# Kernel tuning notes

Hardware: AMD Instinct MI355X
Metric: run time of the kernel (lower is better)

The kernel has to match this reference:

```python
import jax, jax.numpy as jnp
import numpy as np

# yolov5 non_max_suppression defaults (from forward's input_parameters.get defaults)
CONF_THRES = 0.25
IOU_THRES = 0.45
MAX_DET = 1000        # max detections returned per image
TOP_K = 4096          # fixed candidate count entering greedy NMS (jit-friendly stand-in for max_nms)
MAX_WH = 7680.0       # per-class box offset so NMS is class-aware (yolov5 trick)


def setup_inputs() -> dict:
    key = jax.random.key(0)
    k1, k2, k3, k4 = jax.random.split(key, 4)
    B, N, NC = 16, 25200, 80  # 640x640 yolov5 -> 25200 anchors, 80 COCO classes
    xy = jax.random.uniform(k1, (B, N, 2)) * 640.0            # box centers in pixels
    wh = jax.random.uniform(k2, (B, N, 2)) * 160.0 + 4.0       # box sizes
    obj = jax.random.uniform(k3, (B, N, 1))                    # objectness
    cls = jax.random.uniform(k4, (B, N, NC))                   # class scores
    pred = jnp.concatenate([xy, wh, obj, cls], axis=-1)        # [B, N, 85]
    return {"pred": pred}


def _xywh2xyxy(x):
    xy, wh = x[..., :2], x[..., 2:4]
    return jnp.concatenate([xy - wh * 0.5, xy + wh * 0.5], axis=-1)


def _iou_one_vs_all(box, boxes):
    # box [4], boxes [K,4], xyxy
    lt = jnp.maximum(box[:2], boxes[:, :2])
    rb = jnp.minimum(box[2:], boxes[:, 2:])
    wh = jnp.clip(rb - lt, 0.0)
    inter = wh[:, 0] * wh[:, 1]
    a1 = (box[2] - box[0]) * (box[3] - box[1])
    a2 = (boxes[:, 2] - boxes[:, 0]) * (boxes[:, 3] - boxes[:, 1])
    return inter / (a1 + a2 - inter + 1e-7)


def _nms_single(pred):
    # pred [N, 5+nc] raw yolov5 output for one image
    obj = pred[:, 4:5]
    scores_all = pred[:, 5:] * obj                 # conf = obj_conf * cls_conf
    conf = scores_all.max(axis=-1)                 # best-class confidence [N]
    cls = scores_all.argmax(axis=-1).astype(pred.dtype)
    boxes = _xywh2xyxy(pred[:, :4])                # [N,4] xyxy

    valid = conf > CONF_THRES
    s = jnp.where(valid, conf, -1.0)
    order = jnp.argsort(-s)[:TOP_K]                # top candidates by score
    b = boxes[order]                               # [K,4]
    sc = s[order]                                  # [K]
    c = cls[order]                                 # [K]
    ob = b + c[:, None] * MAX_WH                   # class-offset boxes for class-aware NMS

    ar = jnp.arange(TOP_K)

    def step(supp, i):
        alive = (~supp[i]) & (sc[i] > 0.0)
        iou = _iou_one_vs_all(ob[i], ob)
        supp = supp | (alive & (iou > IOU_THRES) & (ar > i))
        return supp, alive

    _, keep = jax.lax.scan(step, jnp.zeros(TOP_K, dtype=bool), ar)

    fs = jnp.where(keep, sc, -1.0)
    idx = jnp.argsort(-fs)[:MAX_DET]               # kept boxes, score-sorted
    det = jnp.concatenate([b[idx], fs[idx][:, None], c[idx][:, None]], axis=-1)  # [max_det,6]
    ok = fs[idx] > 0.0
    return jnp.where(ok[:, None], det, 0.0)        # zero-padded [max_det, 6] (x1,y1,x2,y2,conf,cls)


def reference(pred):
    # [B, max_det, 6] padded detections per image
    return jax.vmap(_nms_single)(pred)
```

## Files before the change

### kernel.cpp

```cpp
#include <hip/hip_runtime.h>

#define BATCH  16
#define NPRED  25200
#define NCLS   80
#define CDIM   85
#define TOPK   4096
#define NBUCK  4096
#define MAXDET 1000
#define CONF_T 0.25f
#define IOU_T  0.45f
#define MAXWH  7680.0f
#define ORD_BASE 0xBE800000u

typedef unsigned long long u64;
typedef unsigned int u32;
typedef unsigned short u16;
typedef unsigned char u8;

__device__ __forceinline__ u64 umax64(u64 a, u64 b) { return a > b ? a : b; }
__device__ __forceinline__ u64 umin64(u64 a, u64 b) { return a < b ? a : b; }

__device__ __forceinline__ void cx_u64(u64* a, int i, int p, bool desc) {
    u64 x = a[i], y = a[p];
    if (desc ? (x < y) : (x > y)) { a[i] = y; a[p] = x; }
}

__device__ __forceinline__ float4 build_box(const float* __restrict__ row, float off) {
    float x = row[0], y = row[1], w = row[2], hh = row[3];
    float4 o;
    o.x = (x - w * 0.5f) + off;
    o.y = (y - hh * 0.5f) + off;
    o.z = (x + w * 0.5f) + off;
    o.w = (y + hh * 0.5f) + off;
    return o;
}


__device__ void hybrid_sort4096_desc_ks(u64 r[4], u64* a, int kstart) {
    const int tid = threadIdx.x;
    for (int k = kstart; k <= 4096; k <<= 1) {
        if (k >= 512) {
            int jmax = (k >> 1) > 2048 ? 2048 : (k >> 1);
#pragma unroll
            for (int e = 0; e < 4; ++e) a[4 * tid + e] = r[e];
            __syncthreads();
            for (int j = jmax; j >= 256; j >>= 1) {
#pragma unroll
                for (int t2 = 0; t2 < 2; ++t2) {
                    int q = (t2 << 10) | tid;
                    int i = ((q & ~(j - 1)) << 1) | (q & (j - 1));
                    cx_u64(a, i, i | j, (i & k) == 0);
                }
                __syncthreads();
            }
#pragma unroll
            for (int e = 0; e < 4; ++e) r[e] = a[4 * tid + e];
            __syncthreads();
        }
        {
            int jstart = (k >> 1) > 128 ? 128 : (k >> 1);
            bool desc = (((4 * tid) & k) == 0);
            for (int j = jstart; j >= 4; j >>= 1) {
                int m = j >> 2;
                bool take_max = (((tid & m) == 0) == desc);
#pragma unroll
                for (int e = 0; e < 4; ++e) {
                    u64 v = __shfl_xor(r[e], m, 64);
                    r[e] = take_max ? umax64(r[e], v) : umin64(r[e], v);
                }
            }
        }
        if (k >= 4) {
            bool desc = (((4 * tid) & k) == 0);
            u64 x0 = r[0], x2 = r[2];
            r[0] = desc ? umax64(x0, x2) : umin64(x0, x2);
            r[2] = desc ? umin64(x0, x2) : umax64(x0, x2);
            u64 x1 = r[1], x3 = r[3];
            r[1] = desc ? umax64(x1, x3) : umin64(x1, x3);
            r[3] = desc ? umin64(x1, x3) : umax64(x1, x3);
        }
        {
            bool d01 = (((4 * tid + 0) & k) == 0);
            bool d23 = (((4 * tid + 2) & k) == 0);
            u64 x0 = r[0], x1 = r[1];
            r[0] = d01 ? umax64(x0, x1) : umin64(x0, x1);
            r[1] = d01 ? umin64(x0, x1) : umax64(x0, x1);
            u64 x2 = r[2], x3 = r[3];
            r[2] = d23 ? umax64(x2, x3) : umin64(x2, x3);
            r[3] = d23 ? umin64(x2, x3) : umax64(x2, x3);
        }
    }
}


__device__ void hybrid_sort1024_dir(u64 r[4], u64* a, bool fdesc) {
    const int tid = threadIdx.x;
    for (int k = 2; k <= 1024; k <<= 1) {
        if (k >= 512) {
            int jmax = (k >> 1) > 512 ? 512 : (k >> 1);
#pragma unroll
            for (int e = 0; e < 4; ++e) a[4 * tid + e] = r[e];
            __syncthreads();
            for (int j = jmax; j >= 256; j >>= 1) {
#pragma unroll
                for (int t2 = 0; t2 < 2; ++t2) {
                    int q = (t2 << 8) | tid;
                    int i = ((q & ~(j - 1)) << 1) | (q & (j - 1));
                    cx_u64(a, i, i | j, ((i & k) == 0) == fdesc);
                }
                __syncthreads();
            }
#pragma unroll
            for (int e = 0; e < 4; ++e) r[e] = a[4 * tid + e];
            __syncthreads();
        }
        {
            int jstart = (k >> 1) > 128 ? 128 : (k >> 1);
            bool desc = ((((4 * tid) & k) == 0) == fdesc);
            for (int j = jstart; j >= 4; j >>= 1) {
                int m = j >> 2;
                bool take_max = (((tid & m) == 0) == desc);
#pragma unroll
                for (int e = 0; e < 4; ++e) {
                    u64 v = __shfl_xor(r[e], m, 64);
                    r[e] = take_max ? umax64(r[e], v) : umin64(r[e], v);
                }
            }
        }
        if (k >= 4) {
            bool desc = ((((4 * tid) & k) == 0) == fdesc);
            u64 x0 = r[0], x2 = r[2];
            r[0] = desc ? umax64(x0, x2) : umin64(x0, x2);
            r[2] = desc ? umin64(x0, x2) : umax64(x0, x2);
            u64 x1 = r[1], x3 = r[3];
            r[1] = desc ? umax64(x1, x3) : umin64(x1, x3);
            r[3] = desc ? umin64(x1, x3) : umax64(x1, x3);
        }
        {
            bool d01 = ((((4 * tid + 0) & k) == 0) == fdesc);
            bool d23 = ((((4 * tid + 2) & k) == 0) == fdesc);
            u64 x0 = r[0], x1 = r[1];
            r[0] = d01 ? umax64(x0, x1) : umin64(x0, x1);
            r[1] = d01 ? umin64(x0, x1) : umax64(x0, x1);
            u64 x2 = r[2], x3 = r[3];
            r[2] = d23 ? umax64(x2, x3) : umin64(x2, x3);
            r[3] = d23 ? umin64(x2, x3) : umax64(x2, x3);
        }
    }
}

__device__ void wave_sort256_desc(u64 r[4]) {
    const int lane = threadIdx.x & 63;
    for (int k = 2; k <= 256; k <<= 1) {
        int jstart = (k >> 1) > 128 ? 128 : (k >> 1);
        bool desc = (((4 * lane) & k) == 0);
        for (int j = jstart; j >= 4; j >>= 1) {
            int m = j >> 2;
            bool take_max = (((lane & m) == 0) == desc);
#pragma unroll
            for (int e = 0; e < 4; ++e) {
                u64 v = __shfl_xor(r[e], m, 64);
                r[e] = take_max ? umax64(r[e], v) : umin64(r[e], v);
            }
        }
        if (k >= 4) {
            u64 x0 = r[0], x2 = r[2];
            r[0] = desc ? umax64(x0, x2) : umin64(x0, x2);
            r[2] = desc ? umin64(x0, x2) : umax64(x0, x2);
            u64 x1 = r[1], x3 = r[3];
            r[1] = desc ? umax64(x1, x3) : umin64(x1, x3);
            r[3] = desc ? umin64(x1, x3) : umax64(x1, x3);
        }
        {
            bool d01 = (((4 * lane + 0) & k) == 0);
            bool d23 = (((4 * lane + 2) & k) == 0);
            u64 x0 = r[0], x1 = r[1];
            r[0] = d01 ? umax64(x0, x1) : umin64(x0, x1);
            r[1] = d01 ? umin64(x0, x1) : umax64(x0, x1);
            u64 x2 = r[2], x3 = r[3];
            r[2] = d23 ? umax64(x2, x3) : umin64(x2, x3);
            r[3] = d23 ? umin64(x2, x3) : umax64(x2, x3);
        }
    }
}


__global__ __launch_bounds__(256) void k1_score(const float* __restrict__ pred,
                                                u64* __restrict__ keys) {
    const int lane = threadIdx.x & 63;
    const int l16 = lane & 15;
    const long long gw = (long long)blockIdx.x * 4 + (threadIdx.x >> 6);
    const long long rowIdx = gw * 4 + (lane >> 4);
    const int b = (int)(rowIdx / NPRED);
    const int n = (int)(rowIdx - (long long)b * NPRED);
    const float* row = pred + rowIdx * CDIM;
    float obj = row[4];
    u64 m = 0ull;
#pragma unroll
    for (int k = 0; k < 5; ++k) {
        int c = l16 + 16 * k;
        float v = row[5 + c] * obj;
        u64 mk = ((u64)(__float_as_uint(v) | 0x80000000u) << 32) | (u64)(u32)(NCLS - 1 - c);
        if (mk > m) m = mk;
    }
#pragma unroll
    for (int o = 8; o > 0; o >>= 1) {
        u64 other = __shfl_xor(m, o, 64);
        if (other > m) m = other;
    }
    if (l16 == 0) {
        float best = __uint_as_float((u32)(m >> 32) & 0x7FFFFFFFu);
        int cls = (NCLS - 1) - (int)(m & 0x7Fu);
        float s = (best > CONF_T) ? best : -1.0f;
        u32 u = __float_as_uint(s);
        u32 ord = (u & 0x80000000u) ? ~u : (u | 0x80000000u);
        keys[rowIdx] = ((u64)ord << 32) | ((u64)(u32)(32767 - n) << 7) | (u64)(u32)cls;
    }
}


__global__ __launch_bounds__(1024) void k2a(const u64* __restrict__ keys,
                                            u64* __restrict__ topUn,
                                            u8* __restrict__ keep) {
    __shared__ u64 smem[4096];
    __shared__ u64 side[1024];
    __shared__ u32 hist[4096];
    __shared__ u32 wsum[16];
    __shared__ int sh_T, sh_C1, sh_R, c1pos, sidepos;
    const int b = blockIdx.x;
    const int tid = threadIdx.x;
    const int lane = tid & 63;
    const int wid = tid >> 6;
    const u64 lanelt = (1ull << lane) - 1ull;

#pragma unroll
    for (int e = 0; e < 4; ++e) { smem[4 * tid + e] = 0ull; hist[4 * tid + e] = 0u; }
    side[tid] = 0ull;
    ((u32*)keep)[b * 1024 + tid] = 0u;
    __syncthreads();

    const u64* kb = keys + (long long)b * NPRED;
    for (int it = 0; it < (NPRED + 1023) / 1024; ++it) {
        int n = it * 1024 + tid;
        if (n < NPRED) {
            u32 hi = (u32)(kb[n] >> 32);
            if (hi > ORD_BASE) atomicAdd(&hist[(hi - ORD_BASE - 1u) >> 12], 1u);
        }
    }
    __syncthreads();

    u32 h[4];
    u32 tsum = 0;
#pragma unroll
    for (int e = 0; e < 4; ++e) {
        h[e] = hist[NBUCK - 1 - (4 * tid + e)];
        tsum += h[e];
    }
    u32 inc = tsum;
    for (int o = 1; o < 64; o <<= 1) {
        u32 v = __shfl_up(inc, o, 64);
        if (lane >= o) inc += v;
    }
    if (lane == 63) wsum[wid] = inc;
    __syncthreads();
    if (tid == 0) {
        u32 run = 0;
        for (int i = 0; i < 16; ++i) { u32 t = wsum[i]; wsum[i] = run; run += t; }
        sh_T = -1; sh_C1 = (int)run; sh_R = 0;
        c1pos = 0; sidepos = 0;
    }
    __syncthreads();
    {
        u32 cum = wsum[wid] + (inc - tsum);
#pragma unroll
        for (int e = 0; e < 4; ++e) {
            if (h[e] > 0 && cum < (u32)TOPK && cum + h[e] >= (u32)TOPK) {
                sh_T = NBUCK - 1 - (4 * tid + e);
                sh_C1 = (int)cum;
                sh_R = TOPK - (int)cum;
            }
            cum += h[e];
        }
    }
    __syncthreads();
    const int T = sh_T, C1 = sh_C1, R = sh_R;

    for (int it = 0; it < (NPRED + 1023) / 1024; ++it) {
        int n = it * 1024 + tid;
        bool act = n < NPRED;
        u64 key = act ? kb[n] : 0ull;
        u32 hi = (u32)(key >> 32);
        bool v = act && (hi > ORD_BASE);
        int bt = v ? (int)((hi - ORD_BASE - 1u) >> 12) : -1;
        bool t1 = v && (bt > T);
        bool t2 = v && (bt == T);
        u64 m1 = __ballot(t1), m2 = __ballot(t2);
        int b1 = 0, b2 = 0;
        if (lane == 0) {
            if (m1) b1 = atomicAdd(&c1pos, (int)__popcll(m1));
            if (m2) b2 = atomicAdd(&sidepos, (int)__popcll(m2));
        }
        b1 = __shfl(b1, 0, 64);
        b2 = __shfl(b2, 0, 64);
        if (t1) smem[b1 + __popcll(m1 & lanelt)] = key;
        if (t2) { int s2 = b2 + __popcll(m2 & lanelt); if (s2 < 1024) side[s2] = key; }
    }
    __syncthreads();

    if (R > 0) {
        int cntT = sidepos;
        if (cntT <= 256) {
            if (wid == 0) {
                u64 r[4];
#pragma unroll
                for (int e = 0; e < 4; ++e) r[e] = side[4 * lane + e];
                wave_sort256_desc(r);
#pragma unroll
                for (int e = 0; e < 4; ++e) side[4 * lane + e] = r[e];
            }
        } else {
            for (int k = 2; k <= 1024; k <<= 1) {
                for (int j = k >> 1; j >= 1; j >>= 1) {
                    if (tid < 512) {
                        int q = tid;
                        int i = ((q & ~(j - 1)) << 1) | (q & (j - 1));
                        cx_u64(side, i, i | j, (i & k) == 0);
                    }
                    __syncthreads();
                }
            }
        }
        __syncthreads();
        if (tid < R) smem[C1 + tid] = side[tid];
    }
    __syncthreads();

    for (int i = tid; i < 4096; i += 1024) topUn[(long long)b * TOPK + i] = smem[i];
}


__global__ __launch_bounds__(256) void k2b(u64* __restrict__ topUn) {
    __shared__ u64 a[1024];
    const int tid = threadIdx.x;
    const int s = blockIdx.x & 3;
    const long long base = (long long)blockIdx.x * 1024;
    u64 r[4];
#pragma unroll
    for (int e = 0; e < 4; ++e) r[e] = topUn[base + 4 * tid + e];
    hybrid_sort1024_dir(r, a, (s & 1) == 0);
#pragma unroll
    for (int e = 0; e < 4; ++e) topUn[base + 4 * tid + e] = r[e];
}


__global__ __launch_bounds__(1024) void k2c(const u64* __restrict__ topUn,
                                            u64* __restrict__ topSorted,
                                            u32* __restrict__ segIdx,
                                            u32* __restrict__ cntg,
                                            u32* __restrict__ startg) {
    __shared__ u64 a[4096];
    __shared__ u32 cnt[NCLS];
    __shared__ u32 startc[NCLS];
    const int b = blockIdx.x;
    const int tid = threadIdx.x;
    const int lane = tid & 63;
    const int wid = tid >> 6;
    const u64 lanelt = (1ull << lane) - 1ull;

    u64 r[4];
#pragma unroll
    for (int e = 0; e < 4; ++e) r[e] = topUn[(long long)b * TOPK + 4 * tid + e];
    hybrid_sort4096_desc_ks(r, a, 2048);
#pragma unroll
    for (int e = 0; e < 4; ++e) topSorted[(long long)b * TOPK + 4 * tid + e] = r[e];

    if (tid < NCLS) cnt[tid] = 0u;
    __syncthreads();
    u32* arr = (u32*)a;
#pragma unroll
    for (int e = 0; e < 4; ++e) {
        int j = 4 * tid + e;
        u64 key = r[e];
        u32 hi = (u32)(key >> 32);
        u32 v = 0x7Fu;
        if (hi > 0x80000000u) {
            u32 np = 32767u - (u32)((key >> 7) & 0x7FFFu);
            v = (u32)(key & 0x7Fu) | (np << 7);
            atomicAdd(&cnt[(int)(key & 0x7Fu)], 1u);
        }
        arr[j] = v;
    }
    __syncthreads();
    if (tid == 0) {
        u32 run = 0;
        for (int c = 0; c < NCLS; ++c) { startc[c] = run; run += cnt[c]; }
    }
    __syncthreads();

    {
        u32 pos0 = startc[wid +  0], pos1 = startc[wid + 16], pos2 = startc[wid + 32],
            pos3 = startc[wid + 48], pos4 = startc[wid + 64];
        u32* sg = segIdx + b * TOPK;
        for (int it = 0; it < 64; ++it) {
            int j = it * 64 + lane;
            u32 aj = arr[j];
            int cc = (int)(aj & 0x7Fu);
            u32 entry = ((u32)j << 15) | (aj >> 7);
            u64 m;
            m = __ballot(cc == wid +  0); if (cc == wid +  0) sg[pos0 + __popcll(m & lanelt)] = entry; pos0 += (u32)__popcll(m);
            m = __ballot(cc == wid + 16); if (cc == wid + 16) sg[pos1 + __popcll(m & lanelt)] = entry; pos1 += (u32)__popcll(m);
            m = __ballot(cc == wid + 32); if (cc == wid + 32) sg[pos2 + __popcll(m & lanelt)] = entry; pos2 += (u32)__popcll(m);
            m = __ballot(cc == wid + 48); if (cc == wid + 48) sg[pos3 + __popcll(m & lanelt)] = entry; pos3 += (u32)__popcll(m);
            m = __ballot(cc == wid + 64); if (cc == wid + 64) sg[pos4 + __popcll(m & lanelt)] = entry; pos4 += (u32)__popcll(m);
        }
    }
    if (tid < NCLS) {
        cntg[b * NCLS + tid] = cnt[tid];
        startg[b * NCLS + tid] = startc[tid];
    }
}


__global__ __launch_bounds__(64) void k3_nms(const float* __restrict__ pred,
                                             const u32* __restrict__ segIdx,
                                             const u32* __restrict__ cntg,
                                             const u32* __restrict__ startg,
                                             u8* __restrict__ keep) {
    const int b = blockIdx.x;
    const int c = blockIdx.y;
    const int lane = threadIdx.x;
    __shared__ u8 suppb[4096];
    const int n = (int)cntg[b * NCLS + c];
    if (n == 0) return;
    const u32 base = startg[b * NCLS + c];
    const u32* seg = segIdx + b * TOPK + base;
    u8* kb = keep + b * TOPK;
    const float off = (float)c * MAXWH;

    if (n <= 128) {
        u32 r0 = 0, r1 = 0;
        float4 b0 = make_float4(0.0f, 0.0f, 0.0f, 0.0f);
        float4 b1 = make_float4(0.0f, 0.0f, 0.0f, 0.0f);
        if (lane < n) {
            u32 e = seg[lane];
            r0 = e >> 15;
            b0 = build_box(pred + ((long long)b * NPRED + (int)(e & 0x7FFFu)) * CDIM, off);
        }
        if (64 + lane < n) {
            u32 e = seg[64 + lane];
            r1 = e >> 15;
            b1 = build_box(pred + ((long long)b * NPRED + (int)(e & 0x7FFFu)) * CDIM, off);
        }
        {
#pragma clang fp contract(off)
            float a20 = (b0.z - b0.x) * (b0.w - b0.y);
            float a21 = (b1.z - b1.x) * (b1.w - b1.y);
            u64 rem0 = (n >= 64) ? ~0ull : ((1ull << n) - 1ull);
            u64 rem1 = (n > 64) ? ((n >= 128) ? ~0ull : ((1ull << (n - 64)) - 1ull)) : 0ull;
            u64 keep0 = 0ull, keep1 = 0ull;
            const bool two = (n > 64);
            while (rem0) {
                int ii = __builtin_ctzll(rem0);
                rem0 &= ~(1ull << ii);
                keep0 |= 1ull << ii;
                float bix = __shfl(b0.x, ii, 64);
                float biy = __shfl(b0.y, ii, 64);
                float biz = __shfl(b0.z, ii, 64);
                float biw = __shfl(b0.w, ii, 64);
                float a1  = __shfl(a20, ii, 64);
                {
                    float ltx = fmaxf(bix, b0.x), lty = fmaxf(biy, b0.y);
                    float rbx = fminf(biz, b0.z), rby = fminf(biw, b0.w);
                    float ww = fmaxf(rbx - ltx, 0.0f), hh = fmaxf(rby - lty, 0.0f);
                    float inter = ww * hh;
                    float iou = inter / (((a1 + a20) - inter) + 1e-7f);
                    bool k0 = (iou > IOU_T) && (lane > ii);
                    rem0 &= ~__ballot(k0);
                }
                if (two) {
                    float ltx = fmaxf(bix, b1.x), lty = fmaxf(biy, b1.y);
                    float rbx = fminf(biz, b1.z), rby = fminf(biw, b1.w);
                    float ww = fmaxf(rbx - ltx, 0.0f), hh = fmaxf(rby - lty, 0.0f);
                    float inter = ww * hh;
                    float iou = inter / (((a1 + a21) - inter) + 1e-7f);
                    bool k1 = (iou > IOU_T);
                    rem1 &= ~__ballot(k1);
                }
            }
            while (rem1) {
                int ii = __builtin_ctzll(rem1);
                rem1 &= ~(1ull << ii);
                keep1 |= 1ull << ii;
                float bix = __shfl(b1.x, ii, 64);
                float biy = __shfl(b1.y, ii, 64);
                float biz = __shfl(b1.z, ii, 64);
                float biw = __shfl(b1.w, ii, 64);
                float a1  = __shfl(a21, ii, 64);
                float ltx = fmaxf(bix, b1.x), lty = fmaxf(biy, b1.y);
                float rbx = fminf(biz, b1.z), rby = fminf(biw, b1.w);
                float ww = fmaxf(rbx - ltx, 0.0f), hh = fmaxf(rby - lty, 0.0f);
                float inter = ww * hh;
                float iou = inter / (((a1 + a21) - inter) + 1e-7f);
                bool k1 = (iou > IOU_T) && (lane > ii);
                rem1 &= ~__ballot(k1);
            }
            if ((keep0 >> lane) & 1ull) kb[r0] = 1;
            if ((keep1 >> lane) & 1ull) kb[r1] = 1;
        }
    } else {
        for (int j = lane; j < n; j += 64) suppb[j] = 0;
        __syncthreads();
        volatile u8* supp = suppb;
        {
#pragma clang fp contract(off)
            for (int ii = 0; ii < n; ++ii) {
                if (supp[ii]) continue;
                u32 ei = seg[ii];
                int ri = (int)(ei >> 15);
                if (lane == 0) kb[ri] = 1;
                float4 bi = build_box(pred + ((long long)b * NPRED + (int)(ei & 0x7FFFu)) * CDIM, off);
                float a1 = (bi.z - bi.x) * (bi.w - bi.y);
                for (int jj = ii + 1 + lane; jj < n; jj += 64) {
                    u32 ej = seg[jj];
                    float4 bj = build_box(pred + ((long long)b * NPRED + (int)(ej & 0x7FFFu)) * CDIM, off);
                    float ltx = fmaxf(bi.x, bj.x), lty = fmaxf(bi.y, bj.y);
                    float rbx = fminf(bi.z, bj.z), rby = fminf(bi.w, bj.w);
                    float ww = fmaxf(rbx - ltx, 0.0f), hh = fmaxf(rby - lty, 0.0f);
                    float inter = ww * hh;
                    float a2 = (bj.z - bj.x) * (bj.w - bj.y);
                    float iou = inter / (((a1 + a2) - inter) + 1e-7f);
                    if (iou > IOU_T) supp[jj] = 1;
                }
                __syncthreads();
            }
        }
    }
}


__global__ __launch_bounds__(256) void k4_out(const float* __restrict__ pred,
                                              const u64* __restrict__ topSorted,
                                              const u8* __restrict__ keep,
                                              float* __restrict__ out) {
    const int b = blockIdx.x;
    const int tid = threadIdx.x;
    __shared__ u64 words[64];
    __shared__ int wpre[64];
    float* outb = out + (long long)b * MAXDET * 6;
    for (int i = tid; i < MAXDET * 6; i += 256) outb[i] = 0.0f;
    const u8* kp = keep + b * 4096;
    if (tid < 64) {
        u64 w = 0ull;
        const u64* k8 = (const u64*)(kp + tid * 64);
#pragma unroll
        for (int q = 0; q < 8; ++q) {
            u64 v = k8[q];
#pragma unroll
            for (int bb = 0; bb < 8; ++bb)
                if ((v >> (8 * bb)) & 0xFFull) w |= 1ull << (q * 8 + bb);
        }
        words[tid] = w;
    }
    __syncthreads();
    if (tid == 0) {
        int run = 0;
        for (int t = 0; t < 64; ++t) { wpre[t] = run; run += __popcll(words[t]); }
    }
    __syncthreads();
    const u64* kb = topSorted + (long long)b * TOPK;
    for (int r = tid; r < 4096; r += 256) {
        int wd = r >> 6;
        if ((words[wd] >> (r & 63)) & 1ull) {
            int pos = wpre[wd] + __popcll(words[wd] & ((1ull << (r & 63)) - 1ull));
            if (pos < MAXDET) {
                u64 key = kb[r];
                u32 hi = (u32)(key >> 32);
                int n = 32767 - (int)((key >> 7) & 0x7FFFu);
                const float* row = pred + ((long long)b * NPRED + n) * CDIM;
                float x = row[0], y = row[1], w2 = row[2], h = row[3];
                float* o = outb + pos * 6;
                o[0] = x - w2 * 0.5f;
                o[1] = y - h * 0.5f;
                o[2] = x + w2 * 0.5f;
                o[3] = y + h * 0.5f;
                o[4] = __uint_as_float(hi & 0x7FFFFFFFu);
                o[5] = (float)(key & 0x7Fu);
            }
        }
    }
}


extern "C" void kernel_launch(void* const* d_in, const int* in_sizes, int n_in,
                              void* d_out, int out_size, void* d_ws, size_t ws_size,
                              hipStream_t stream) {
    const float* pred = (const float*)d_in[0];
    float* out = (float*)d_out;

    char* ws = (char*)d_ws;
    u64* keys      = (u64*)ws;
    u64* topUn     = (u64*)(ws + 3225600);
    u64* topSorted = (u64*)(ws + 3749888);
    u32* segIdx    = (u32*)(ws + 4274176);
    u32* cntg      = (u32*)(ws + 4536320);
    u32* startg    = (u32*)(ws + 4541440);
    u8*  keep      = (u8*)(ws + 4546560);

    hipLaunchKernelGGL(k1_score, dim3(BATCH * NPRED / 16), dim3(256), 0, stream,
                       pred, keys);
    hipLaunchKernelGGL(k2a, dim3(BATCH), dim3(1024), 0, stream, keys, topUn, keep);
    hipLaunchKernelGGL(k2b, dim3(BATCH * 4), dim3(256), 0, stream, topUn);
    hipLaunchKernelGGL(k2c, dim3(BATCH), dim3(1024), 0, stream, topUn, topSorted,
                       segIdx, cntg, startg);
    hipLaunchKernelGGL(k3_nms, dim3(BATCH, NCLS), dim3(64), 0, stream,
                       pred, segIdx, cntg, startg, keep);
    hipLaunchKernelGGL(k4_out, dim3(BATCH), dim3(256), 0, stream, pred, topSorted, keep, out);
}
```

Baseline: 276.6 us.

## Fuse top-K selection and both sort stages into one kernel per image

Merges the three kernels k2a, k2b and k2c into a single kernel with one 1024-thread block per image. The selected candidates stay in shared memory: four 256-thread groups each sort a 1024-element chunk in alternating directions, then the block-wide 4096 merge sort runs in place. This removes two kernel launches and the global round-trips through the topUn buffer. In exchange, the 1024-chunk sorts now run on only 16 blocks instead of 64, so less of the GPU works on that phase. The block barriers inside the group sort are now shared by all four groups.

Measured after the change: 281.2 us. About the same (+1.7%).

```diff
diff --git a/kernel.cpp b/kernel.cpp
--- a/kernel.cpp
+++ b/kernel.cpp
@@ -93,33 +93,32 @@
 }
 
 
-__device__ void hybrid_sort1024_dir(u64 r[4], u64* a, bool fdesc) {
-    const int tid = threadIdx.x;
+__device__ void group_sort1024_dir(u64 r[4], u64* a, int gtid, bool fdesc) {
     for (int k = 2; k <= 1024; k <<= 1) {
         if (k >= 512) {
             int jmax = (k >> 1) > 512 ? 512 : (k >> 1);
 #pragma unroll
-            for (int e = 0; e < 4; ++e) a[4 * tid + e] = r[e];
+            for (int e = 0; e < 4; ++e) a[4 * gtid + e] = r[e];
             __syncthreads();
             for (int j = jmax; j >= 256; j >>= 1) {
 #pragma unroll
                 for (int t2 = 0; t2 < 2; ++t2) {
-                    int q = (t2 << 8) | tid;
+                    int q = (t2 << 8) | gtid;
                     int i = ((q & ~(j - 1)) << 1) | (q & (j - 1));
                     cx_u64(a, i, i | j, ((i & k) == 0) == fdesc);
                 }
                 __syncthreads();
             }
 #pragma unroll
-            for (int e = 0; e < 4; ++e) r[e] = a[4 * tid + e];
+            for (int e = 0; e < 4; ++e) r[e] = a[4 * gtid + e];
             __syncthreads();
         }
         {
             int jstart = (k >> 1) > 128 ? 128 : (k >> 1);
-            bool desc = ((((4 * tid) & k) == 0) == fdesc);
+            bool desc = ((((4 * gtid) & k) == 0) == fdesc);
             for (int j = jstart; j >= 4; j >>= 1) {
                 int m = j >> 2;
-                bool take_max = (((tid & m) == 0) == desc);
+                bool take_max = (((gtid & m) == 0) == desc);
 #pragma unroll
                 for (int e = 0; e < 4; ++e) {
                     u64 v = __shfl_xor(r[e], m, 64);
@@ -128,7 +127,7 @@
             }
         }
         if (k >= 4) {
-            bool desc = ((((4 * tid) & k) == 0) == fdesc);
+            bool desc = ((((4 * gtid) & k) == 0) == fdesc);
             u64 x0 = r[0], x2 = r[2];
             r[0] = desc ? umax64(x0, x2) : umin64(x0, x2);
             r[2] = desc ? umin64(x0, x2) : umax64(x0, x2);
@@ -137,8 +136,8 @@
             r[3] = desc ? umin64(x1, x3) : umax64(x1, x3);
         }
         {
-            bool d01 = ((((4 * tid + 0) & k) == 0) == fdesc);
-            bool d23 = ((((4 * tid + 2) & k) == 0) == fdesc);
+            bool d01 = ((((4 * gtid + 0) & k) == 0) == fdesc);
+            bool d23 = ((((4 * gtid + 2) & k) == 0) == fdesc);
             u64 x0 = r[0], x1 = r[1];
             r[0] = d01 ? umax64(x0, x1) : umin64(x0, x1);
             r[1] = d01 ? umin64(x0, x1) : umax64(x0, x1);
@@ -219,13 +218,18 @@
 }
 
 
-__global__ __launch_bounds__(1024) void k2a(const u64* __restrict__ keys,
-                                            u64* __restrict__ topUn,
-                                            u8* __restrict__ keep) {
+__global__ __launch_bounds__(1024) void k2_sel(const u64* __restrict__ keys,
+                                               u64* __restrict__ topSorted,
+                                               u32* __restrict__ segIdx,
+                                               u32* __restrict__ cntg,
+                                               u32* __restrict__ startg,
+                                               u8* __restrict__ keep) {
     __shared__ u64 smem[4096];
     __shared__ u64 side[1024];
     __shared__ u32 hist[4096];
     __shared__ u32 wsum[16];
+    __shared__ u32 cnt[NCLS];
+    __shared__ u32 startc[NCLS];
     __shared__ int sh_T, sh_C1, sh_R, c1pos, sidepos;
     const int b = blockIdx.x;
     const int tid = threadIdx.x;
@@ -335,48 +339,22 @@
     }
     __syncthreads();
 
-    for (int i = tid; i < 4096; i += 1024) topUn[(long long)b * TOPK + i] = smem[i];
-}
-
-
-__global__ __launch_bounds__(256) void k2b(u64* __restrict__ topUn) {
-    __shared__ u64 a[1024];
-    const int tid = threadIdx.x;
-    const int s = blockIdx.x & 3;
-    const long long base = (long long)blockIdx.x * 1024;
     u64 r[4];
-#pragma unroll
-    for (int e = 0; e < 4; ++e) r[e] = topUn[base + 4 * tid + e];
-    hybrid_sort1024_dir(r, a, (s & 1) == 0);
-#pragma unroll
-    for (int e = 0; e < 4; ++e) topUn[base + 4 * tid + e] = r[e];
-}
-
-
-__global__ __launch_bounds__(1024) void k2c(const u64* __restrict__ topUn,
-                                            u64* __restrict__ topSorted,
-                                            u32* __restrict__ segIdx,
-                                            u32* __restrict__ cntg,
-                                            u32* __restrict__ startg) {
-    __shared__ u64 a[4096];
-    __shared__ u32 cnt[NCLS];
-    __shared__ u32 startc[NCLS];
-    const int b = blockIdx.x;
-    const int tid = threadIdx.x;
-    const int lane = tid & 63;
-    const int wid = tid >> 6;
-    const u64 lanelt = (1ull << lane) - 1ull;
-
-    u64 r[4];
-#pragma unroll
-    for (int e = 0; e < 4; ++e) r[e] = topUn[(long long)b * TOPK + 4 * tid + e];
-    hybrid_sort4096_desc_ks(r, a, 2048);
-#pragma unroll
-    for (int e = 0; e < 4; ++e) topSorted[(long long)b * TOPK + 4 * tid + e] = r[e];
+    {
+        const int g = tid >> 8;
+        const int gtid = tid & 255;
+        u64* ga = smem + (g << 10);
+#pragma unroll
+        for (int e = 0; e < 4; ++e) r[e] = ga[4 * gtid + e];
+        group_sort1024_dir(r, ga, gtid, (g & 1) == 0);
+        hybrid_sort4096_desc_ks(r, smem, 2048);
+#pragma unroll
+        for (int e = 0; e < 4; ++e) topSorted[(long long)b * TOPK + 4 * tid + e] = r[e];
+    }
 
     if (tid < NCLS) cnt[tid] = 0u;
     __syncthreads();
-    u32* arr = (u32*)a;
+    u32* arr = (u32*)smem;
 #pragma unroll
     for (int e = 0; e < 4; ++e) {
         int j = 4 * tid + e;
@@ -599,19 +577,16 @@
 
     char* ws = (char*)d_ws;
     u64* keys      = (u64*)ws;
-    u64* topUn     = (u64*)(ws + 3225600);
-    u64* topSorted = (u64*)(ws + 3749888);
-    u32* segIdx    = (u32*)(ws + 4274176);
-    u32* cntg      = (u32*)(ws + 4536320);
-    u32* startg    = (u32*)(ws + 4541440);
-    u8*  keep      = (u8*)(ws + 4546560);
+    u64* topSorted = (u64*)(ws + 3225600);
+    u32* segIdx    = (u32*)(ws + 3749888);
+    u32* cntg      = (u32*)(ws + 4012032);
+    u32* startg    = (u32*)(ws + 4017152);
+    u8*  keep      = (u8*)(ws + 4022272);
 
     hipLaunchKernelGGL(k1_score, dim3(BATCH * NPRED / 16), dim3(256), 0, stream,
                        pred, keys);
-    hipLaunchKernelGGL(k2a, dim3(BATCH), dim3(1024), 0, stream, keys, topUn, keep);
-    hipLaunchKernelGGL(k2b, dim3(BATCH * 4), dim3(256), 0, stream, topUn);
-    hipLaunchKernelGGL(k2c, dim3(BATCH), dim3(1024), 0, stream, topUn, topSorted,
-                       segIdx, cntg, startg);
+    hipLaunchKernelGGL(k2_sel, dim3(BATCH), dim3(1024), 0, stream,
+                       keys, topSorted, segIdx, cntg, startg, keep);
     hipLaunchKernelGGL(k3_nms, dim3(BATCH, NCLS), dim3(64), 0, stream,
                        pred, segIdx, cntg, startg, keep);
     hipLaunchKernelGGL(k4_out, dim3(BATCH), dim3(256), 0, stream, pred, topSorted, keep, out);
```
